# Kernel tuning notes

Hardware: AMD Instinct MI355X
Metric: run time of the kernel (lower is better)

## Reference

```python
import jax, jax.numpy as jnp
import numpy as np

E, D_IN, D_HID, D_OUT, B = 8, 128, 256, 128, 65536


def setup_inputs() -> dict:
    key = jax.random.key(0)
    ks = jax.random.split(key, 6)
    s1 = 1.0 / np.sqrt(D_IN)
    s2 = 1.0 / np.sqrt(D_HID)
    return {
        "x": jax.random.normal(ks[0], (B, D_IN), dtype=jnp.float32),
        "weights": jax.random.uniform(ks[1], (B, E), dtype=jnp.float32),
        "W1": jax.random.uniform(ks[2], (E, D_IN, D_HID), jnp.float32, -s1, s1),
        "b1": jax.random.uniform(ks[3], (E, D_HID), jnp.float32, -s1, s1),
        "W2": jax.random.uniform(ks[4], (E, D_HID, D_OUT), jnp.float32, -s2, s2),
        "b2": jax.random.uniform(ks[5], (E, D_OUT), jnp.float32, -s2, s2),
    }


def reference(x, weights, W1, b1, W2, b2):
    # all-experts dense MLP: every expert processes the full batch
    h = jax.nn.relu(jnp.einsum("bi,eih->beh", x, W1) + b1[None])  # [B,E,H]
    y = jnp.einsum("beh,eho->beo", h, W2) + b2[None]              # [B,E,O]
    # weighted combine over experts
    return jnp.einsum("beo,be->bo", y, weights)                   # [B,O]
```

## Files before the change

### kernel.cpp

```cpp
#include <hip/hip_runtime.h>


#define E_    8
#define DIN_  128
#define DH_   256
#define DOUT_ 128
#define BM_   128
#define NCHUNK 32
#define REC1  18432

typedef __attribute__((ext_vector_type(8))) short bf16x8;
typedef __attribute__((ext_vector_type(16))) float f32x16;
typedef __attribute__((ext_vector_type(2))) unsigned int uint2v;

__device__ __forceinline__ unsigned short f2bf(float f) {
  union { float f; unsigned int u; } v; v.f = f;
  unsigned int u = v.u;
  u += 0x7fffu + ((u >> 16) & 1u);
  return (unsigned short)(u >> 16);
}

__device__ __forceinline__ unsigned int cvt_pk_bf16(float lo, float hi) {
  unsigned int r;
  asm("v_cvt_pk_bf16_f32 %0, %1, %2" : "=v"(r) : "v"(lo), "v"(hi));
  return r;
}

__device__ __forceinline__ bf16x8 pack4(unsigned int a, unsigned int b,
                                        unsigned int c, unsigned int d) {
  union { unsigned int u[4]; bf16x8 v; } t;
  t.u[0] = a; t.u[1] = b; t.u[2] = c; t.u[3] = d;
  return t.v;
}

__device__ __forceinline__ void gload_lds16(const void* g, void* l) {
  __builtin_amdgcn_global_load_lds(
      (const __attribute__((address_space(1))) unsigned int*)g,
      (__attribute__((address_space(3))) unsigned int*)l, 16, 0, 0);
}

__global__ __launch_bounds__(256) void prep_w1(
    const float* __restrict__ W1, const float* __restrict__ b1,
    unsigned char* __restrict__ W1r)
{
  __shared__ float T[8192];
  const int t = blockIdx.x;
  const int e = t >> 2, hc = t & 3;
  const int tid = threadIdx.x;
  unsigned char* rec = W1r + (size_t)t * REC1;

  #pragma unroll
  for (int i = 0; i < 32; ++i) {
    int idx = i * 256 + tid;
    int k = idx >> 6, c = idx & 63;
    T[idx] = W1[((size_t)(e * DIN_ + k)) * DH_ + hc * 64 + c];
  }
  __syncthreads();
  #pragma unroll
  for (int j = 0; j < 16; ++j) {
    int widx = j * 256 + tid;
    int c = widx >> 6, uw = (widx & 63) * 4;
    int up = uw ^ ((c & 7) << 4);
    int k0 = up >> 1;
    unsigned int val = (unsigned int)f2bf(T[k0 * 64 + c]) |
                       ((unsigned int)f2bf(T[(k0 + 1) * 64 + c]) << 16);
    *(unsigned int*)(rec + c * 256 + uw) = val;
  }
  if (tid < 64) {
    *(unsigned int*)(rec + 16384 + tid * 32) =
        (unsigned int)f2bf(b1[e * DH_ + hc * 64 + tid]);
    #pragma unroll
    for (int p = 1; p < 8; ++p)
      *(unsigned int*)(rec + 16384 + tid * 32 + p * 4) = 0u;
  }
}

__global__ __launch_bounds__(256) void prep_w2p(
    const float* __restrict__ W2, unsigned int* __restrict__ W2p)
{
  const int t = blockIdx.x;
  const int e = t >> 2, hc = t & 3;
  const int tid = threadIdx.x;
  unsigned int* outw = W2p + (size_t)t * 4096;
  #pragma unroll
  for (int j = 0; j < 16; ++j) {
    int w = j * 256 + tid;
    int wh = w >> 11, k2 = (w >> 10) & 1, nf = (w >> 8) & 3;
    int lane = (w >> 2) & 63, pr = w & 3;
    int hi = lane >> 5, l32 = lane & 31;
    int n = nf * 32 + l32;
    int c = hc * 64 + wh * 32 + k2 * 16 + hi * 8 + pr * 2;
    unsigned int val =
        (unsigned int)f2bf(W2[((size_t)(e * DH_ + c)) * DOUT_ + n]) |
        ((unsigned int)f2bf(W2[((size_t)(e * DH_ + c + 1)) * DOUT_ + n]) << 16);
    outw[w] = val;
  }
}

__global__ __launch_bounds__(256, 2) void moe_main(
    const float* __restrict__ x, const float* __restrict__ wts,
    const float* __restrict__ b2, const unsigned char* __restrict__ W1r,
    const unsigned char* __restrict__ W2p, float* __restrict__ out)
{
  __shared__ __align__(16) unsigned char L[2][REC1];

  const int tid  = threadIdx.x;
  const int lane = tid & 63;
  const int wv   = tid >> 6;
  const int l32  = lane & 31;
  const int hi   = lane >> 5;
  const int swz  = (l32 & 7) << 4;
  const long bm  = (long)blockIdx.x * BM_;
  const long m   = bm + wv * 32 + l32;

  auto stage = [&](int t, unsigned char* dst) {
    const unsigned char* src = W1r + (size_t)t * REC1;
    #pragma unroll
    for (int r = 0; r < 4; ++r)
      gload_lds16(src + (r * 256 + tid) * 16, dst + r * 4096 + wv * 1024);
    if (tid < 128)
      gload_lds16(src + 16384 + tid * 16, dst + 16384 + wv * 1024);
  };

  stage(0, L[0]);

  int p1o[8];
  #pragma unroll
  for (int ks = 0; ks < 8; ++ks)
    p1o[ks] = l32 * 256 + ((ks * 32 + hi * 16) ^ swz);
  const int bo = 16384 + l32 * 32 + hi * 16;

  const bf16x8 ones = pack4(hi ? 0u : 0x3F80u, 0u, 0u, 0u);

  float wreg[8];
  {
    float4 a = *(const float4*)(wts + m * E_);
    float4 b = *(const float4*)(wts + m * E_ + 4);
    wreg[0] = a.x; wreg[1] = a.y; wreg[2] = a.z; wreg[3] = a.w;
    wreg[4] = b.x; wreg[5] = b.y; wreg[6] = b.z; wreg[7] = b.w;
  }

  bf16x8 xf[8];
  #pragma unroll
  for (int ks = 0; ks < 8; ++ks) {
    const float* xr = x + m * DIN_ + ks * 16 + hi * 8;
    float4 a = *(const float4*)xr;
    float4 b = *(const float4*)(xr + 4);
    xf[ks] = pack4(cvt_pk_bf16(a.x, a.y), cvt_pk_bf16(a.z, a.w),
                   cvt_pk_bf16(b.x, b.y), cvt_pk_bf16(b.z, b.w));
  }

  f32x16 oacc[4];
  #pragma unroll
  for (int nf = 0; nf < 4; ++nf) oacc[nf] = 0.0f;

  auto compute = [&](const unsigned char* Lb, int t, bf16x8* w2f) {
    const int e = t >> 2;
    const float w = wreg[e];
    bf16x8 bfr0 = *(const bf16x8*)(Lb + bo);
    bf16x8 bfr1 = *(const bf16x8*)(Lb + bo + 1024);

    f32x16 h0 = 0.0f, h1 = 0.0f;
    __builtin_amdgcn_s_setprio(1);
    #pragma unroll
    for (int ks = 0; ks < 8; ++ks) {
      bf16x8 a0 = *(const bf16x8*)(Lb + p1o[ks]);
      bf16x8 a1 = *(const bf16x8*)(Lb + p1o[ks] + 8192);
      h0 = __builtin_amdgcn_mfma_f32_32x32x16_bf16(a0, xf[ks], h0, 0, 0, 0);
      h1 = __builtin_amdgcn_mfma_f32_32x32x16_bf16(a1, xf[ks], h1, 0, 0, 0);
    }
    h0 = __builtin_amdgcn_mfma_f32_32x32x16_bf16(bfr0, ones, h0, 0, 0, 0);
    h1 = __builtin_amdgcn_mfma_f32_32x32x16_bf16(bfr1, ones, h1, 0, 0, 0);
    __builtin_amdgcn_s_setprio(0);

    bf16x8 hfr[4];
    #pragma unroll
    for (int cf = 0; cf < 2; ++cf) {
      const f32x16& hh = cf ? h1 : h0;
      unsigned int u[8];
      #pragma unroll
      for (int p = 0; p < 8; ++p) {
        float a = fmaxf(hh[2 * p],     0.0f) * w;
        float b = fmaxf(hh[2 * p + 1], 0.0f) * w;
        u[p] = cvt_pk_bf16(a, b);
      }
      uint2v s02 = __builtin_amdgcn_permlane32_swap(u[0], u[2], false, false);
      uint2v s13 = __builtin_amdgcn_permlane32_swap(u[1], u[3], false, false);
      uint2v s46 = __builtin_amdgcn_permlane32_swap(u[4], u[6], false, false);
      uint2v s57 = __builtin_amdgcn_permlane32_swap(u[5], u[7], false, false);
      hfr[2 * cf]     = pack4(s02[0], s13[0], s02[1], s13[1]);
      hfr[2 * cf + 1] = pack4(s46[0], s57[0], s46[1], s57[1]);
    }

    __builtin_amdgcn_s_setprio(1);
    #pragma unroll
    for (int kk = 0; kk < 4; ++kk) {
      #pragma unroll
      for (int nf = 0; nf < 4; ++nf) {
        bf16x8 b = w2f[(kk >> 1) * 8 + (kk & 1) * 4 + nf];
        oacc[nf] = __builtin_amdgcn_mfma_f32_32x32x16_bf16(hfr[kk], b, oacc[nf], 0, 0, 0);
      }
    }
    __builtin_amdgcn_s_setprio(0);
  };

  for (int tt = 0; tt < NCHUNK; tt += 2) {
    __syncthreads();
    {
      bf16x8 w2f[16];
      const unsigned char* wb = W2p + (size_t)tt * 16384 + lane * 16;
      #pragma unroll
      for (int i = 0; i < 16; ++i)
        w2f[i] = *(const bf16x8*)(wb + i * 1024);
      stage(tt + 1, L[1]);
      compute(&L[0][0], tt, w2f);
    }
    __syncthreads();
    {
      bf16x8 w2f[16];
      const unsigned char* wb = W2p + (size_t)(tt + 1) * 16384 + lane * 16;
      #pragma unroll
      for (int i = 0; i < 16; ++i)
        w2f[i] = *(const bf16x8*)(wb + i * 1024);
      if (tt + 2 < NCHUNK) stage(tt + 2, L[0]);
      compute(&L[1][0], tt + 1, w2f);
    }
  }

  const unsigned int z = 0;
  bf16x8 wfrag = pack4(hi ? z : cvt_pk_bf16(wreg[0], wreg[1]),
                       hi ? z : cvt_pk_bf16(wreg[2], wreg[3]),
                       hi ? z : cvt_pk_bf16(wreg[4], wreg[5]),
                       hi ? z : cvt_pk_bf16(wreg[6], wreg[7]));
  #pragma unroll
  for (int nf = 0; nf < 4; ++nf) {
    const float* bp = b2 + nf * 32 + l32;
    bf16x8 bfrag = pack4(
        hi ? z : cvt_pk_bf16(bp[0 * DOUT_], bp[1 * DOUT_]),
        hi ? z : cvt_pk_bf16(bp[2 * DOUT_], bp[3 * DOUT_]),
        hi ? z : cvt_pk_bf16(bp[4 * DOUT_], bp[5 * DOUT_]),
        hi ? z : cvt_pk_bf16(bp[6 * DOUT_], bp[7 * DOUT_]));
    oacc[nf] = __builtin_amdgcn_mfma_f32_32x32x16_bf16(wfrag, bfrag, oacc[nf], 0, 0, 0);
  }

  #pragma unroll
  for (int nf = 0; nf < 4; ++nf) {
    #pragma unroll
    for (int r = 0; r < 16; ++r) {
      const int mloc = (r & 3) + 8 * (r >> 2) + 4 * hi;
      out[(bm + wv * 32 + mloc) * DOUT_ + nf * 32 + l32] = oacc[nf][r];
    }
  }
}

extern "C" void kernel_launch(void* const* d_in, const int* in_sizes, int n_in,
                              void* d_out, int out_size, void* d_ws, size_t ws_size,
                              hipStream_t stream) {
  const float* x   = (const float*)d_in[0];
  const float* wts = (const float*)d_in[1];
  const float* W1  = (const float*)d_in[2];
  const float* b1  = (const float*)d_in[3];
  const float* W2  = (const float*)d_in[4];
  const float* b2  = (const float*)d_in[5];
  float* out = (float*)d_out;

  unsigned char* W1r = (unsigned char*)d_ws;
  unsigned char* W2p = W1r + (size_t)NCHUNK * REC1;

  prep_w1<<<32, 256, 0, stream>>>(W1, b1, W1r);
  prep_w2p<<<32, 256, 0, stream>>>(W2, (unsigned int*)W2p);
  moe_main<<<65536 / BM_, 256, 0, stream>>>(x, wts, b2, W1r, W2p, out);
}
```

Before: 103.3 us.

## Replace syncthreads double-buffer loop with explicit vmcnt waits and wider LDS swizzle

The main loop now runs one chunk per iteration with raw s_barrier plus hand-placed s_waitcnt vmcnt counts. Only the previous stage's LDS loads have to land before compute, so the W2 register loads and the next stage's prefetch stay in flight. The W1 record grows to 20480 bytes and is staged by five uniform 16-byte loads per thread, and the XOR swizzle widens from 8 to 16 rows to cut LDS bank conflicts. This costs more LDS per block, and the correctness of the hard-coded vmcnt values depends on the exact order of instructions the compiler emits.

New measurement: 102.7 us. No clear change (-0.5%).

```diff
diff --git a/kernel.cpp b/kernel.cpp
--- a/kernel.cpp
+++ b/kernel.cpp
@@ -7,7 +7,7 @@
 #define DOUT_ 128
 #define BM_   128
 #define NCHUNK 32
-#define REC1  18432
+#define REC1  20480
 
 typedef __attribute__((ext_vector_type(8))) short bf16x8;
 typedef __attribute__((ext_vector_type(16))) float f32x16;
@@ -60,7 +60,7 @@
   for (int j = 0; j < 16; ++j) {
     int widx = j * 256 + tid;
     int c = widx >> 6, uw = (widx & 63) * 4;
-    int up = uw ^ ((c & 7) << 4);
+    int up = uw ^ ((c & 15) << 4);
     int k0 = up >> 1;
     unsigned int val = (unsigned int)f2bf(T[k0 * 64 + c]) |
                        ((unsigned int)f2bf(T[(k0 + 1) * 64 + c]) << 16);
@@ -109,25 +109,23 @@
   const int wv   = tid >> 6;
   const int l32  = lane & 31;
   const int hi   = lane >> 5;
-  const int swz  = (l32 & 7) << 4;
+  const int swz4 = (l32 & 15) << 4;
   const long bm  = (long)blockIdx.x * BM_;
   const long m   = bm + wv * 32 + l32;
 
   auto stage = [&](int t, unsigned char* dst) {
     const unsigned char* src = W1r + (size_t)t * REC1;
     #pragma unroll
-    for (int r = 0; r < 4; ++r)
+    for (int r = 0; r < 5; ++r)
       gload_lds16(src + (r * 256 + tid) * 16, dst + r * 4096 + wv * 1024);
-    if (tid < 128)
-      gload_lds16(src + 16384 + tid * 16, dst + 16384 + wv * 1024);
   };
 
-  stage(0, L[0]);
+  stage(0, &L[0][0]);
 
   int p1o[8];
   #pragma unroll
   for (int ks = 0; ks < 8; ++ks)
-    p1o[ks] = l32 * 256 + ((ks * 32 + hi * 16) ^ swz);
+    p1o[ks] = l32 * 256 + ((ks * 32 + hi * 16) ^ swz4);
   const int bo = 16384 + l32 * 32 + hi * 16;
 
   const bf16x8 ones = pack4(hi ? 0u : 0x3F80u, 0u, 0u, 0u);
@@ -204,27 +202,29 @@
     __builtin_amdgcn_s_setprio(0);
   };
 
-  for (int tt = 0; tt < NCHUNK; tt += 2) {
-    __syncthreads();
+  int cur = 0;
+  for (int t = 0; t < NCHUNK; ++t) {
+    __builtin_amdgcn_s_barrier();
+    __builtin_amdgcn_sched_barrier(0);
+    bf16x8 w2f[16];
     {
-      bf16x8 w2f[16];
-      const unsigned char* wb = W2p + (size_t)tt * 16384 + lane * 16;
+      const unsigned char* wb = W2p + (size_t)t * 16384 + lane * 16;
       #pragma unroll
       for (int i = 0; i < 16; ++i)
         w2f[i] = *(const bf16x8*)(wb + i * 1024);
-      stage(tt + 1, L[1]);
-      compute(&L[0][0], tt, w2f);
-    }
-    __syncthreads();
-    {
-      bf16x8 w2f[16];
-      const unsigned char* wb = W2p + (size_t)(tt + 1) * 16384 + lane * 16;
-      #pragma unroll
-      for (int i = 0; i < 16; ++i)
-        w2f[i] = *(const bf16x8*)(wb + i * 1024);
-      if (tt + 2 < NCHUNK) stage(tt + 2, L[0]);
-      compute(&L[1][0], tt + 1, w2f);
-    }
+    }
+    if (t + 1 < NCHUNK) {
+      stage(t + 1, &L[cur ^ 1][0]);
+      __builtin_amdgcn_sched_barrier(0);
+      asm volatile("s_waitcnt vmcnt(21)" ::: "memory");
+    } else {
+      __builtin_amdgcn_sched_barrier(0);
+      asm volatile("s_waitcnt vmcnt(16)" ::: "memory");
+    }
+    __builtin_amdgcn_s_barrier();
+    __builtin_amdgcn_sched_barrier(0);
+    compute(&L[cur][0], t, w2f);
+    cur ^= 1;
   }
 
   const unsigned int z = 0;
```
